# Kernel tuning notes

Measured on AMD Instinct MI355X. Metric: run time of the kernel, lower is better.

The kernel has to match this reference:

```python
import jax, jax.numpy as jnp
import numpy as np

EPS = 1e-5
NEG_SLOPE = 0.1


def conv2d(x, w, b, pad):
    y = jax.lax.conv_general_dilated(x, w, (1, 1), ((pad[0], pad[0]), (pad[1], pad[1])),
                                     dimension_numbers=('NCHW', 'OIHW', 'NCHW'))
    return y + b[None, :, None, None]


def bn(x, g, b, m, v):
    # inference-mode BatchNorm2d
    scale = g / jnp.sqrt(v + EPS)
    return (x - m[None, :, None, None]) * scale[None, :, None, None] + b[None, :, None, None]


def leaky(x):
    return jnp.where(x >= 0, x, NEG_SLOPE * x)


def pos_embed(C, T, V):
    # STTFormer-style sinusoidal embedding over joint index, repeated per frame
    pos = jnp.tile(jnp.arange(V, dtype=jnp.float32), T)[:, None]            # (T*V, 1)
    div = jnp.exp(jnp.arange(0, C, 2, dtype=jnp.float32) * (-np.log(10000.0) / C))
    pe = jnp.zeros((T * V, C), jnp.float32)
    pe = pe.at[:, 0::2].set(jnp.sin(pos * div)).at[:, 1::2].set(jnp.cos(pos * div))
    return pe.reshape(T, V, C).transpose(2, 0, 1)[None]                      # (1, C, T, V)


def ema(x, c1w, c1b, c3w, c3b, gng, gnb, groups):
    # Efficient Multi-scale Attention (EMA) module
    b, c, h, w = x.shape
    cg = c // groups
    gx = x.reshape(b * groups, cg, h, w)
    x_h = gx.mean(axis=3, keepdims=True)                                     # (bg, cg, h, 1)
    x_w = jnp.swapaxes(gx.mean(axis=2, keepdims=True), 2, 3)                 # (bg, cg, w, 1)
    hw = conv2d(jnp.concatenate([x_h, x_w], axis=2), c1w, c1b, (0, 0))       # 1x1 conv
    xh, xw = hw[:, :, :h], hw[:, :, h:]
    g = gx * jax.nn.sigmoid(xh) * jax.nn.sigmoid(jnp.swapaxes(xw, 2, 3))
    # GroupNorm(cg, cg): one channel per group -> per-channel spatial norm
    mu = g.mean((2, 3), keepdims=True)
    var = g.var((2, 3), keepdims=True)
    x1 = (g - mu) / jnp.sqrt(var + EPS) * gng[None, :, None, None] + gnb[None, :, None, None]
    x2 = conv2d(gx, c3w, c3b, (1, 1))                                        # 3x3 conv
    x11 = jax.nn.softmax(x1.mean((2, 3))[:, None, :], axis=-1)               # (bg, 1, cg)
    x21 = jax.nn.softmax(x2.mean((2, 3))[:, None, :], axis=-1)
    x12 = x2.reshape(b * groups, cg, h * w)
    x22 = x1.reshape(b * groups, cg, h * w)
    weights = (x11 @ x12 + x21 @ x22).reshape(b * groups, 1, h, w)
    return (gx * jax.nn.sigmoid(weights)).reshape(b, c, h, w)


def _forward(x, atten_weight, qkv_w, qkv_b, alphas, att0s, nets_w, nets_b,
             bn1_g, bn1_b, bn1_m, bn1_v,
             e1_c1w, e1_c1b, e1_c3w, e1_c3b, e1_gng, e1_gnb,
             bn2_g, bn2_b, bn2_m, bn2_v,
             nett_w, nett_b, bn3_g, bn3_b, bn3_m, bn3_v,
             e2_c1w, e2_c1b, e2_c3w, e2_c3b, e2_gng, e2_gnb,
             bn4_g, bn4_b, bn4_m, bn4_v):
    N, C, T, V = x.shape
    H = alphas.shape[1]
    D = qkv_w.shape[0] // (2 * H)
    xs = pos_embed(C, T, V) + x
    # 1x1 conv to q,k
    qk = jnp.einsum('oc,nctv->notv', qkv_w, xs) + qkv_b[None, :, None, None]
    qk = qk.reshape(N, 2 * H, D, T, V)
    q, k = qk[:, :H], qk[:, H:]
    # tanh attention over joints (V x V), scaled, weighted, plus learned bias table
    att = jnp.tanh(jnp.einsum('nhctu,nhctv->nhuv', q, k) / (D * T)) * alphas
    att = att * atten_weight[None, None] + att0s
    xs = jnp.einsum('nctu,nhuv->nhctv', x, att).reshape(N, H * C, T, V)
    x_ress = x  # in_channels == out_channels -> identity residual
    xs = leaky(bn(conv2d(xs, nets_w, nets_b, (0, 1)), bn1_g, bn1_b, bn1_m, bn1_v) + x_ress)
    xs = leaky(bn(ema(xs, e1_c1w, e1_c1b, e1_c3w, e1_c3b, e1_gng, e1_gnb, 16),
                  bn2_g, bn2_b, bn2_m, bn2_v) + x_ress)
    xt = leaky(bn(conv2d(xs, nett_w, nett_b, (2, 0)), bn3_g, bn3_b, bn3_m, bn3_v) + xs)
    xt = leaky(bn(ema(xt, e2_c1w, e2_c1b, e2_c3w, e2_c3b, e2_gng, e2_gnb, 32),
                  bn4_g, bn4_b, bn4_m, bn4_v) + xs)
    return xt


def setup_inputs() -> dict:
    key = jax.random.key(0)
    N, C, T, V, H, D, O = 64, 64, 120, 25, 3, 64, 64
    cg1, cg2 = O // 16, O // 32
    ks = jax.random.split(key, 16)
    f32 = jnp.float32

    def bn_params(k, c):
        k1, k2 = jax.random.split(k)
        return (jnp.ones(c, f32), jnp.zeros(c, f32),
                jax.random.normal(k1, (c,), f32) * 0.1,
                jax.random.uniform(k2, (c,), f32) + 0.5)

    bn1 = bn_params(ks[5], O)
    bn2 = bn_params(ks[6], O)
    bn3 = bn_params(ks[7], O)
    bn4 = bn_params(ks[8], O)
    return {
        'x': jax.random.normal(ks[0], (N, C, T, V), f32),
        'atten_weight': jax.random.uniform(ks[1], (V, V), f32),
        'qkv_w': jax.random.normal(ks[2], (2 * H * D, C), f32) * 0.05,
        'qkv_b': jnp.zeros(2 * H * D, f32),
        'alphas': jnp.ones((1, H, 1, 1), f32),
        'att0s': jnp.ones((1, H, V, V), f32) / V,
        'nets_w': jax.random.normal(ks[3], (O, C * H, 1, 3), f32) * 0.05,
        'nets_b': jnp.zeros(O, f32),
        'bn1_g': bn1[0], 'bn1_b': bn1[1], 'bn1_m': bn1[2], 'bn1_v': bn1[3],
        'e1_c1w': jax.random.normal(ks[9], (cg1, cg1, 1, 1), f32) * 0.1,
        'e1_c1b': jnp.zeros(cg1, f32),
        'e1_c3w': jax.random.normal(ks[10], (cg1, cg1, 3, 3), f32) * 0.1,
        'e1_c3b': jnp.zeros(cg1, f32),
        'e1_gng': jnp.ones(cg1, f32), 'e1_gnb': jnp.zeros(cg1, f32),
        'bn2_g': bn2[0], 'bn2_b': bn2[1], 'bn2_m': bn2[2], 'bn2_v': bn2[3],
        'nett_w': jax.random.normal(ks[4], (O, O, 5, 1), f32) * 0.05,
        'nett_b': jnp.zeros(O, f32),
        'bn3_g': bn3[0], 'bn3_b': bn3[1], 'bn3_m': bn3[2], 'bn3_v': bn3[3],
        'e2_c1w': jax.random.normal(ks[11], (cg2, cg2, 1, 1), f32) * 0.1,
        'e2_c1b': jnp.zeros(cg2, f32),
        'e2_c3w': jax.random.normal(ks[12], (cg2, cg2, 3, 3), f32) * 0.1,
        'e2_c3b': jnp.zeros(cg2, f32),
        'e2_gng': jnp.ones(cg2, f32), 'e2_gnb': jnp.zeros(cg2, f32),
        'bn4_g': bn4[0], 'bn4_b': bn4[1], 'bn4_m': bn4[2], 'bn4_v': bn4[3],
    }


def reference(x, atten_weight, qkv_w, qkv_b, alphas, att0s, nets_w, nets_b,
              bn1_g, bn1_b, bn1_m, bn1_v,
              e1_c1w, e1_c1b, e1_c3w, e1_c3b, e1_gng, e1_gnb,
              bn2_g, bn2_b, bn2_m, bn2_v,
              nett_w, nett_b, bn3_g, bn3_b, bn3_m, bn3_v,
              e2_c1w, e2_c1b, e2_c3w, e2_c3b, e2_gng, e2_gnb,
              bn4_g, bn4_b, bn4_m, bn4_v):
    return _forward(x, atten_weight, qkv_w, qkv_b, alphas, att0s, nets_w, nets_b,
                    bn1_g, bn1_b, bn1_m, bn1_v,
                    e1_c1w, e1_c1b, e1_c3w, e1_c3b, e1_gng, e1_gnb,
                    bn2_g, bn2_b, bn2_m, bn2_v,
                    nett_w, nett_b, bn3_g, bn3_b, bn3_m, bn3_v,
                    e2_c1w, e2_c1b, e2_c3w, e2_c3b, e2_gng, e2_gnb,
                    bn4_g, bn4_b, bn4_m, bn4_v)
```

## Files before the change

kernel.cpp:

```cpp
#include <hip/hip_runtime.h>

typedef float v2f __attribute__((ext_vector_type(2)));
typedef float v4f __attribute__((ext_vector_type(4)));
__device__ __forceinline__ v2f mk2(float a, float b){ v2f r; r.x=a; r.y=b; return r; }
__device__ __forceinline__ v2f bc2(float x){ v2f r; r.x=x; r.y=x; return r; }

__device__ __forceinline__ float sigm(float x){ return 1.f/(1.f+__expf(-x)); }

__device__ __forceinline__ float waveReduceSum(float v){
  #pragma unroll
  for (int o = 32; o > 0; o >>= 1) v += __shfl_down(v, o, 64);
  return v;
}
__device__ __forceinline__ float blockReduceSum(float v, float* red4, int tid){
  v = waveReduceSum(v);
  __syncthreads();
  if ((tid & 63) == 0) red4[tid >> 6] = v;
  __syncthreads();
  return red4[0] + red4[1] + red4[2] + red4[3];
}

__global__ __launch_bounds__(256) void zeroS_kernel(float* __restrict__ S){
  int i = blockIdx.x*256 + threadIdx.x;
  if (i < 120000) S[i] = 0.f;
}

__global__ __launch_bounds__(256) void att_prep_kernel(
    const float* __restrict__ qkv_w, const float* __restrict__ qkv_b, float* __restrict__ Mbuf)
{
  const int h = blockIdx.x;
  const int tid = threadIdx.x;
  __shared__ float Wq[4096], Wk[4096];
  for (int i=tid;i<4096;i+=256){
    Wq[i] = qkv_w[(size_t)h*4096 + i];
    Wk[i] = qkv_w[(size_t)(3+h)*4096 + i];
  }
  __syncthreads();
  int c = tid>>2, cp0 = (tid&3)*16;
  float acc[16];
  #pragma unroll
  for (int j=0;j<16;j++) acc[j]=0.f;
  for (int cq=0;cq<64;cq++){
    float wq = Wq[cq*64+c];
    #pragma unroll
    for (int j=0;j<16;j++) acc[j] += wq*Wk[cq*64+cp0+j];
  }
  float* dst = Mbuf + (size_t)h*4352;
  #pragma unroll
  for (int j=0;j<16;j++) dst[(cp0+j)*68 + c] = acc[j];
  if (tid < 128){
    int row = tid>>6, cp = tid&63;
    const float* W = row ? Wq : Wk;
    const float* bvec = qkv_b + (row ? h*64 : (3+h)*64);
    const float* bb = row ? (qkv_b + (3+h)*64) : (qkv_b + h*64);
    float s=0;
    for (int cq=0;cq<64;cq++) s += bb[cq]*W[cq*64+cp];
    Mbuf[(size_t)h*4352 + cp*68 + 64 + row] = s;
    (void)bvec;
  }
  if (tid==0){
    const float* qb = qkv_b + h*64; const float* kb = qkv_b + (3+h)*64;
    float s=0;
    for (int i=0;i<64;i++) s += qb[i]*kb[i];
    Mbuf[13056 + h] = s;
  }
}

__global__ __launch_bounds__(256,4) void att_partial_kernel(
    const float* __restrict__ x, const float* __restrict__ Mbuf, float* __restrict__ S)
{
  const int nh = blockIdx.x;
  const int tc = blockIdx.y;
  const int n = nh / 3, h = nh % 3;
  const int tid = threadIdx.x;
  __shared__ __align__(16) float Ms[4352];
  __shared__ float xt[1600];
  __shared__ float Ybuf[1650];
  for (int i=tid;i<4352;i+=256) Ms[i] = Mbuf[(size_t)h*4352 + i];

  float pe_reg[7]; int goff[7];
  #pragma unroll
  for (int k=0;k<7;k++){
    int i = tid + k*256;
    if (i < 1600){
      int c = i/25, uu = i%25;
      float freq = __expf(-(float)(2*(c>>1)) * 0.14391156835f);
      float a = (float)uu * freq;
      pe_reg[k] = (c & 1) ? cosf(a) : sinf(a);
      goff[k] = (n*64 + c)*3000 + uu;
    }
  }
  v2f saccv[2] = { {0.f,0.f}, {0.f,0.f} };
  float sacc4 = 0.f;
  const int u = tid / 5, v0 = (tid % 5) * 5;
  const int yc0 = (tid/25)*8, yv = tid%25;
  const int xv = (tid-200)%25;

  for (int t = tc*15; t < tc*15 + 15; ++t){
    __syncthreads();
    #pragma unroll
    for (int k=0;k<7;k++){
      int i = tid + k*256;
      if (i < 1600) xt[i] = x[goff[k] + t*25] + pe_reg[k];
    }
    __syncthreads();
    if (tid < 200){
      v2f a[4];
      #pragma unroll
      for (int j=0;j<4;j++) a[j] = bc2(0.f);
      const float* xb = &xt[yv];
      #pragma unroll 8
      for (int cp=0; cp<64; ++cp){
        v4f m0 = *reinterpret_cast<const v4f*>(&Ms[cp*68 + yc0]);
        v4f m1 = *reinterpret_cast<const v4f*>(&Ms[cp*68 + yc0 + 4]);
        v2f xv2 = bc2(xb[cp*25]);
        a[0] += mk2(m0.x, m0.y) * xv2;
        a[1] += mk2(m0.z, m0.w) * xv2;
        a[2] += mk2(m1.x, m1.y) * xv2;
        a[3] += mk2(m1.z, m1.w) * xv2;
      }
      #pragma unroll
      for (int j=0;j<4;j++){
        Ybuf[(yc0+2*j)*25 + yv]   = a[j].x;
        Ybuf[(yc0+2*j+1)*25 + yv] = a[j].y;
      }
    } else if (tid < 225){
      v2f a64 = bc2(0.f);
      const float* xb = &xt[xv];
      #pragma unroll 8
      for (int cp=0; cp<64; ++cp){
        v2f m = *reinterpret_cast<const v2f*>(&Ms[cp*68 + 64]);
        a64 += m * bc2(xb[cp*25]);
      }
      Ybuf[64*25 + xv] = a64.x;
      Ybuf[65*25 + xv] = a64.y;
    }
    __syncthreads();
    if (tid < 125){
      const float* Qb = &xt[u];
      const float* Kb = &Ybuf[v0];
      #pragma unroll 8
      for (int c = 0; c < 64; ++c){
        float q = Qb[c*25];
        saccv[0] += bc2(q) * mk2(Kb[c*25+0], Kb[c*25+1]);
        saccv[1] += bc2(q) * mk2(Kb[c*25+2], Kb[c*25+3]);
        sacc4 += q * Kb[c*25+4];
      }
      float ybu = Ybuf[65*25 + u];
      const float* av = &Ybuf[64*25 + v0];
      saccv[0] += mk2(av[0]+ybu, av[1]+ybu);
      saccv[1] += mk2(av[2]+ybu, av[3]+ybu);
      sacc4    += av[4]+ybu;
    }
  }
  if (tid < 125){
    float* dst = S + (size_t)nh*625 + u*25 + v0;
    atomicAdd(dst + 0, saccv[0].x);
    atomicAdd(dst + 1, saccv[0].y);
    atomicAdd(dst + 2, saccv[1].x);
    atomicAdd(dst + 3, saccv[1].y);
    atomicAdd(dst + 4, sacc4);
  }
}

__global__ __launch_bounds__(256) void att_finalize_kernel(
    float* __restrict__ S, const float* __restrict__ attw,
    const float* __restrict__ alphas, const float* __restrict__ att0s,
    const float* __restrict__ c0buf)
{
  int idx = blockIdx.x*256 + threadIdx.x;
  if (idx >= 120000) return;
  int nh = idx / 625, uv = idx % 625;
  int h = nh % 3;
  float a = tanhf((S[idx] + 120.f*c0buf[h]) * (1.f/7680.f)) * alphas[h];
  S[idx] = a * attw[uv] + att0s[h*625 + uv];
}

__global__ __launch_bounds__(256,4) void stage1_kernel(
    const float* __restrict__ x, const float* __restrict__ att,
    const float* __restrict__ nets_w, const float* __restrict__ nets_b,
    const float* __restrict__ bng, const float* __restrict__ bnb,
    const float* __restrict__ bnm, const float* __restrict__ bnv,
    float* __restrict__ s1)
{
  __shared__ float smem[7872];
  float* sc    = smem;
  float* sh    = smem + 64;
  float* att_s = smem + 128;
  float* xts   = smem + 2003;
  float* xbp   = smem + 5267;
  const int n = blockIdx.x, t0 = blockIdx.y*2;
  const int tid = threadIdx.x;

  for (int i=tid;i<1875;i+=256) att_s[i] = att[(size_t)n*1875 + i];
  for (int i=tid;i<3200;i+=256){
    int c=i/50, r=i%50;
    xts[c*51 + r] = x[((size_t)(n*64+c)*120 + t0 + r/25)*25 + (r%25)];
  }
  if (tid < 192){
    int row=tid>>2, p=tid&3;
    xbp[row*54 + ((p&1)?26:0) + ((p>>1)?27:0)] = 0.f;
  }
  if (tid < 64){
    float s = bng[tid]*rsqrtf(bnv[tid]+1e-5f);
    sc[tid]=s; sh[tid]=bnb[tid]-bnm[tid]*s;
  }
  __syncthreads();

  const int op = tid>>3, r = tid&7, tt = r>>2, vq = r&3;
  const int o0 = op*2, v0q = vq*7, nv = (vq<3)?7:4;
  v2f accv[7];
  #pragma unroll
  for (int j=0;j<7;j++) accv[j] = bc2(0.f);

  for (int q=0; q<4; ++q){
    const int hc0 = q*48;
    if (tid < 240){
      int hcH = tid % 48, vg = tid / 48;
      int hc = hc0 + hcH;
      int h = hc>>6, c = hc&63, v0 = vg*5;
      v2f av[5];
      #pragma unroll
      for (int j=0;j<5;j++) av[j] = bc2(0.f);
      const float* xr0 = &xts[c*51];
      for (int u=0;u<25;u++){
        v2f xv = mk2(xr0[u], xr0[u+25]);
        const float* ap = &att_s[(h*25+u)*25 + v0];
        #pragma unroll
        for (int j=0;j<5;j++) av[j] += bc2(ap[j]) * xv;
      }
      #pragma unroll
      for (int j=0;j<5;j++){
        xbp[hcH*54 + 1 + v0 + j]  = av[j].x;
        xbp[hcH*54 + 28 + v0 + j] = av[j].y;
      }
    }
    __syncthreads();

    const float* xbase = &xbp[tt*27 + v0q];
    const float* wg0 = nets_w + (size_t)o0*576 + hc0*3;
    const float* wg1 = wg0 + 576;
    #pragma unroll 4
    for (int hcL=0; hcL<48; ++hcL){
      float xr[9];
      #pragma unroll
      for (int j=0;j<9;j++) xr[j] = xbase[hcL*54 + j];
      v2f w0 = mk2(wg0[hcL*3+0], wg1[hcL*3+0]);
      v2f w1 = mk2(wg0[hcL*3+1], wg1[hcL*3+1]);
      v2f w2 = mk2(wg0[hcL*3+2], wg1[hcL*3+2]);
      #pragma unroll
      for (int j=0;j<7;j++)
        accv[j] += w0*bc2(xr[j]) + w1*bc2(xr[j+1]) + w2*bc2(xr[j+2]);
    }
    __syncthreads();
  }

  float b0 = nets_b[o0], b1 = nets_b[o0+1];
  const int t = t0 + tt;
  #pragma unroll
  for (int j=0;j<7;j++){
    if (j < nv){
      int v = v0q + j;
      size_t base0 = ((size_t)(n*64+o0)*120 + t)*25 + v;
      size_t base1 = ((size_t)(n*64+o0+1)*120 + t)*25 + v;
      float y0 = (accv[j].x + b0)*sc[o0]   + sh[o0]   + x[base0];
      float y1 = (accv[j].y + b1)*sc[o0+1] + sh[o0+1] + x[base1];
      y0 = (y0>=0.f)? y0 : 0.1f*y0;
      y1 = (y1>=0.f)? y1 : 0.1f*y1;
      s1[base0] = y0;
      s1[base1] = y1;
    }
  }
}

__global__ __launch_bounds__(256) void stage3_kernel(
    const float* __restrict__ s2, const float* __restrict__ nett_w, const float* __restrict__ nett_b,
    const float* __restrict__ bng, const float* __restrict__ bnb,
    const float* __restrict__ bnm, const float* __restrict__ bnv,
    float* __restrict__ s3)
{
  const int n = blockIdx.x, t0 = blockIdx.y*4;
  const int tid = threadIdx.x;
  __shared__ float tile[12800];
  __shared__ float sc[64], sh[64];
  for (int i=tid;i<12800;i+=256){
    int c=i/200, r=i%200, tt=r/25, v=r%25;
    int t = t0 + tt - 2;
    tile[i] = (t>=0 && t<120) ? s2[((size_t)(n*64+c)*120 + t)*25 + v] : 0.f;
  }
  if (tid < 64){
    float s = bng[tid]*rsqrtf(bnv[tid]+1e-5f);
    sc[tid]=s; sh[tid]=bnb[tid]-bnm[tid]*s;
  }
  __syncthreads();
  for (int task=tid; task<800; task+=256){
    int og = task/25, v = task%25; int o0 = og*2;
    v2f accv[4];
    { v2f b = mk2(nett_b[o0], nett_b[o0+1]);
      #pragma unroll
      for (int k=0;k<4;k++) accv[k]=b; }
    const float* tb = &tile[v];
    const float* wbase = nett_w + (size_t)o0*320;
    #pragma unroll 4
    for (int c=0;c<64;c++){
      float xr[8];
      #pragma unroll
      for (int k=0;k<8;k++) xr[k] = tb[c*200 + k*25];
      v2f w[5];
      #pragma unroll
      for (int d=0;d<5;d++) w[d] = mk2(wbase[c*5 + d], wbase[320 + c*5 + d]);
      #pragma unroll
      for (int k=0;k<4;k++){
        #pragma unroll
        for (int d=0;d<5;d++) accv[k] += w[d]*bc2(xr[k+d]);
      }
    }
    #pragma unroll
    for (int k=0;k<4;k++){
      int t=t0+k;
      float r0 = tile[o0*200     + (k+2)*25 + v];
      float r1 = tile[(o0+1)*200 + (k+2)*25 + v];
      float y0 = accv[k].x*sc[o0]   + sh[o0]   + r0;
      float y1 = accv[k].y*sc[o0+1] + sh[o0+1] + r1;
      y0 = (y0>=0.f)? y0 : 0.1f*y0;
      y1 = (y1>=0.f)? y1 : 0.1f*y1;
      s3[((size_t)(n*64+o0)*120   + t)*25 + v] = y0;
      s3[((size_t)(n*64+o0+1)*120 + t)*25 + v] = y1;
    }
  }
}

template<int CG, int G>
__global__ __launch_bounds__(256) void ema_kernel(
    const float* __restrict__ in, const float* __restrict__ res,
    const float* __restrict__ c1w, const float* __restrict__ c1b,
    const float* __restrict__ c3w, const float* __restrict__ c3b,
    const float* __restrict__ gng, const float* __restrict__ gnb,
    const float* __restrict__ bng, const float* __restrict__ bnb,
    const float* __restrict__ bnm, const float* __restrict__ bnv,
    float* __restrict__ out)
{
  constexpr int PR = 122*27;
  __shared__ float gx[CG*PR];
  __shared__ float xh[CG*120], xw[CG*25];
  __shared__ float sigh[CG*120], sigw[CG*25];
  __shared__ float red4[4];
  __shared__ float c1w_s[CG*CG], c1b_s[CG], c3w_s[CG*CG*9], c3b_s[CG],
                   gng_s[CG], gnb_s[CG], sc_s[CG], sh_s[CG];
  const int tid = threadIdx.x;
  const int b = blockIdx.x; const int n = b / G; const int grp = b % G; const int c0 = grp*CG;
  const float* src = in + (size_t)(n*64 + c0)*3000;
  for (int i = tid; i < CG*PR; i += 256) gx[i] = 0.f;
  if (tid < CG*CG) c1w_s[tid] = c1w[tid];
  if (tid < CG*CG*9) c3w_s[tid] = c3w[tid];
  if (tid < CG){
    c1b_s[tid] = c1b[tid];
    c3b_s[tid] = c3b[tid]; gng_s[tid]=gng[tid]; gnb_s[tid]=gnb[tid];
    float s = bng[c0+tid] * rsqrtf(bnv[c0+tid]+1e-5f);
    sc_s[tid] = s; sh_s[tid] = bnb[c0+tid] - bnm[c0+tid]*s;
  }
  __syncthreads();
  for (int i = tid; i < CG*3000; i += 256){
    int cc = i/3000, p = i%3000, t = p/25, v = p%25;
    gx[cc*PR + (t+1)*27 + (v+1)] = src[i];
  }
  __syncthreads();
  for (int j = tid; j < CG*120; j += 256){
    int cc=j/120, t=j%120; float s=0;
    for (int v=0;v<25;v++) s += gx[cc*PR+(t+1)*27+(v+1)];
    xh[j] = s*(1.f/25.f);
  }
  for (int j = tid; j < CG*25; j += 256){
    int cc=j/25, v=j%25; float s=0;
    for (int t=0;t<120;t++) s += gx[cc*PR+(t+1)*27+(v+1)];
    xw[j] = s*(1.f/120.f);
  }
  __syncthreads();
  for (int j = tid; j < CG*120; j += 256){
    int cc=j/120, t=j%120; float s=c1b_s[cc];
    #pragma unroll
    for (int i=0;i<CG;i++) s += c1w_s[cc*CG+i]*xh[i*120+t];
    sigh[j] = sigm(s);
  }
  for (int j = tid; j < CG*25; j += 256){
    int cc=j/25, v=j%25; float s=c1b_s[cc];
    #pragma unroll
    for (int i=0;i<CG;i++) s += c1w_s[cc*CG+i]*xw[i*25+v];
    sigw[j] = sigm(s);
  }
  __syncthreads();
  float gs[CG], gss[CG];
  #pragma unroll
  for (int cc=0;cc<CG;cc++){ gs[cc]=0.f; gss[cc]=0.f; }
  for (int p = tid; p < 3000; p += 256){
    int t=p/25, v=p%25;
    #pragma unroll
    for (int cc=0;cc<CG;cc++){
      float g = gx[cc*PR+(t+1)*27+(v+1)]*sigh[cc*120+t]*sigw[cc*25+v];
      gs[cc]+=g; gss[cc]+=g*g;
    }
  }
  #pragma unroll
  for (int cc=0;cc<CG;cc++){
    gs[cc]  = blockReduceSum(gs[cc],  red4, tid);
    gss[cc] = blockReduceSum(gss[cc], red4, tid);
  }
  float mu[CG], inv[CG];
  #pragma unroll
  for (int cc=0;cc<CG;cc++){
    mu[cc] = gs[cc]*(1.f/3000.f);
    float var = gss[cc]*(1.f/3000.f) - mu[cc]*mu[cc];
    inv[cc] = rsqrtf(fmaxf(var, 0.f) + 1e-5f);
  }
  float x11[CG];
  { float mx = gnb_s[0];
    #pragma unroll
    for (int cc=1;cc<CG;cc++) mx = fmaxf(mx, gnb_s[cc]);
    float sum=0;
    #pragma unroll
    for (int cc=0;cc<CG;cc++){ x11[cc]=__expf(gnb_s[cc]-mx); sum+=x11[cc]; }
    float r = 1.f/sum;
    #pragma unroll
    for (int cc=0;cc<CG;cc++) x11[cc]*=r; }
  float Sall[CG];
  #pragma unroll
  for (int i=0;i<CG;i++){ float s=0; for (int t=0;t<120;t++) s += xh[i*120+t]; Sall[i]=s*25.f; }
  float m2[CG];
  #pragma unroll
  for (int cc=0;cc<CG;cc++){
    float acc = c3b_s[cc]*3000.f;
    #pragma unroll
    for (int i=0;i<CG;i++){
      #pragma unroll
      for (int dy=0;dy<3;dy++){
        #pragma unroll
        for (int dx=0;dx<3;dx++){
          float w = c3w_s[(cc*CG+i)*9+dy*3+dx];
          float ss = Sall[i];
          int re = -1, ce = -1;
          if (dy==0){ ss -= 25.f*xh[i*120+119]; re=119; }
          else if (dy==2){ ss -= 25.f*xh[i*120+0]; re=0; }
          if (dx==0){ ss -= 120.f*xw[i*25+24]; ce=24; }
          else if (dx==2){ ss -= 120.f*xw[i*25+0]; ce=0; }
          if (re>=0 && ce>=0) ss += gx[i*PR + (re+1)*27 + (ce+1)];
          acc += w*ss;
        }
      }
    }
    m2[cc] = acc*(1.f/3000.f);
  }
  float x21[CG];
  { float mx = m2[0];
    #pragma unroll
    for (int cc=1;cc<CG;cc++) mx = fmaxf(mx, m2[cc]);
    float sum=0;
    #pragma unroll
    for (int cc=0;cc<CG;cc++){ x21[cc]=__expf(m2[cc]-mx); sum+=x21[cc]; }
    float r = 1.f/sum;
    #pragma unroll
    for (int cc=0;cc<CG;cc++) x21[cc]*=r; }
  float wm[CG*9]; float bm=0.f, kc=0.f;
  #pragma unroll
  for (int k=0;k<CG*9;k++){
    float s=0;
    #pragma unroll
    for (int cc=0;cc<CG;cc++) s += x11[cc]*c3w_s[cc*CG*9 + k];
    wm[k]=s;
  }
  float ga[CG];
  #pragma unroll
  for (int cc=0;cc<CG;cc++){
    bm += x11[cc]*c3b_s[cc];
    ga[cc] = x21[cc]*gng_s[cc]*inv[cc];
    kc += x21[cc]*(gnb_s[cc] - mu[cc]*gng_s[cc]*inv[cc]);
  }
  const float base = bm + kc;
  for (int p = tid; p < 3000; p += 256){
    int t=p/25, v=p%25;
    float wsum = base;
    #pragma unroll
    for (int i=0;i<CG;i++){
      const float* gp = &gx[i*PR + t*27 + v];
      wsum += wm[i*9+0]*gp[0]  + wm[i*9+1]*gp[1]  + wm[i*9+2]*gp[2]
            + wm[i*9+3]*gp[27] + wm[i*9+4]*gp[28] + wm[i*9+5]*gp[29]
            + wm[i*9+6]*gp[54] + wm[i*9+7]*gp[55] + wm[i*9+8]*gp[56];
    }
    #pragma unroll
    for (int cc=0;cc<CG;cc++){
      float g = gx[cc*PR+(t+1)*27+(v+1)]*sigh[cc*120+t]*sigw[cc*25+v];
      wsum += ga[cc]*g;
    }
    float sw = sigm(wsum);
    #pragma unroll
    for (int cc=0;cc<CG;cc++){
      float val = gx[cc*PR+(t+1)*27+(v+1)]*sw;
      float y = val*sc_s[cc] + sh_s[cc] + res[(size_t)(n*64+c0+cc)*3000 + p];
      y = (y >= 0.f) ? y : 0.1f*y;
      out[(size_t)(n*64+c0+cc)*3000 + p] = y;
    }
  }
}

extern "C" void kernel_launch(void* const* d_in, const int* in_sizes, int n_in,
                              void* d_out, int out_size, void* d_ws, size_t ws_size,
                              hipStream_t stream)
{
  const float* x      = (const float*)d_in[0];
  const float* attw   = (const float*)d_in[1];
  const float* qkv_w  = (const float*)d_in[2];
  const float* qkv_b  = (const float*)d_in[3];
  const float* alphas = (const float*)d_in[4];
  const float* att0s  = (const float*)d_in[5];
  const float* nets_w = (const float*)d_in[6];
  const float* nets_b = (const float*)d_in[7];
  const float* bn1g = (const float*)d_in[8];  const float* bn1b = (const float*)d_in[9];
  const float* bn1m = (const float*)d_in[10]; const float* bn1v = (const float*)d_in[11];
  const float* e1c1w = (const float*)d_in[12]; const float* e1c1b = (const float*)d_in[13];
  const float* e1c3w = (const float*)d_in[14]; const float* e1c3b = (const float*)d_in[15];
  const float* e1gng = (const float*)d_in[16]; const float* e1gnb = (const float*)d_in[17];
  const float* bn2g = (const float*)d_in[18]; const float* bn2b = (const float*)d_in[19];
  const float* bn2m = (const float*)d_in[20]; const float* bn2v = (const float*)d_in[21];
  const float* nettw = (const float*)d_in[22]; const float* nettb = (const float*)d_in[23];
  const float* bn3g = (const float*)d_in[24]; const float* bn3b = (const float*)d_in[25];
  const float* bn3m = (const float*)d_in[26]; const float* bn3v = (const float*)d_in[27];
  const float* e2c1w = (const float*)d_in[28]; const float* e2c1b = (const float*)d_in[29];
  const float* e2c3w = (const float*)d_in[30]; const float* e2c3b = (const float*)d_in[31];
  const float* e2gng = (const float*)d_in[32]; const float* e2gnb = (const float*)d_in[33];
  const float* bn4g = (const float*)d_in[34]; const float* bn4b = (const float*)d_in[35];
  const float* bn4m = (const float*)d_in[36]; const float* bn4v = (const float*)d_in[37];

  float* S    = (float*)d_ws;
  float* outf = (float*)d_out;
  float* xbuf = (float*)d_in[0];
  float* Mbuf = (float*)d_out;

  att_prep_kernel<<<3,256,0,stream>>>(qkv_w, qkv_b, Mbuf);
  zeroS_kernel<<<469,256,0,stream>>>(S);
  att_partial_kernel<<<dim3(192,8),256,0,stream>>>(x, Mbuf, S);
  att_finalize_kernel<<<469,256,0,stream>>>(S, attw, alphas, att0s, Mbuf + 13056);
  stage1_kernel<<<dim3(64,60),256,0,stream>>>(x, S, nets_w, nets_b, bn1g,bn1b,bn1m,bn1v, outf);
  ema_kernel<4,16><<<1024,256,0,stream>>>(outf, x,
      e1c1w,e1c1b,e1c3w,e1c3b,e1gng,e1gnb, bn2g,bn2b,bn2m,bn2v, xbuf);
  stage3_kernel<<<dim3(64,30),256,0,stream>>>(xbuf, nettw, nettb, bn3g,bn3b,bn3m,bn3v, outf);
  ema_kernel<2,32><<<2048,256,0,stream>>>(outf, xbuf,
      e2c1w,e2c1b,e2c3w,e2c3b,e2gng,e2gnb, bn4g,bn4b,bn4m,bn4v, outf);
}
```

Before: 992.4 us.

## Double-buffer attention input staging and vectorize conv weight loads

In the attention partial-score kernel, the x tile is now double-buffered. The global load and positional-embedding add for step t+1 overlap the score accumulation of step t, which cuts one barrier per time step. In the temporal/spatial conv kernel, weight reads are grouped into 128-bit vector loads of 12 floats per output channel for every 4 input channels. The double buffer adds 6.4KB of shared memory per block, which may reduce occupancy. The vector loads assume the weight pointers are 16-byte aligned.

```diff
diff --git a/kernel.cpp b/kernel.cpp
--- a/kernel.cpp
+++ b/kernel.cpp
@@ -51,12 +51,10 @@
   if (tid < 128){
     int row = tid>>6, cp = tid&63;
     const float* W = row ? Wq : Wk;
-    const float* bvec = qkv_b + (row ? h*64 : (3+h)*64);
     const float* bb = row ? (qkv_b + (3+h)*64) : (qkv_b + h*64);
     float s=0;
     for (int cq=0;cq<64;cq++) s += bb[cq]*W[cq*64+cp];
     Mbuf[(size_t)h*4352 + cp*68 + 64 + row] = s;
-    (void)bvec;
   }
   if (tid==0){
     const float* qb = qkv_b + h*64; const float* kb = qkv_b + (3+h)*64;
@@ -74,7 +72,7 @@
   const int n = nh / 3, h = nh % 3;
   const int tid = threadIdx.x;
   __shared__ __align__(16) float Ms[4352];
-  __shared__ float xt[1600];
+  __shared__ float xt[2][1600];
   __shared__ float Ybuf[1650];
   for (int i=tid;i<4352;i+=256) Ms[i] = Mbuf[(size_t)h*4352 + i];
 
@@ -96,19 +94,19 @@
   const int yc0 = (tid/25)*8, yv = tid%25;
   const int xv = (tid-200)%25;
 
-  for (int t = tc*15; t < tc*15 + 15; ++t){
-    __syncthreads();
+  auto do_stage = [&](int t, float* dst){
     #pragma unroll
     for (int k=0;k<7;k++){
       int i = tid + k*256;
-      if (i < 1600) xt[i] = x[goff[k] + t*25] + pe_reg[k];
-    }
-    __syncthreads();
+      if (i < 1600) dst[i] = x[goff[k] + t*25] + pe_reg[k];
+    }
+  };
+  auto do_Y = [&](const float* xtb){
     if (tid < 200){
       v2f a[4];
       #pragma unroll
       for (int j=0;j<4;j++) a[j] = bc2(0.f);
-      const float* xb = &xt[yv];
+      const float* xb = &xtb[yv];
       #pragma unroll 8
       for (int cp=0; cp<64; ++cp){
         v4f m0 = *reinterpret_cast<const v4f*>(&Ms[cp*68 + yc0]);
@@ -126,7 +124,7 @@
       }
     } else if (tid < 225){
       v2f a64 = bc2(0.f);
-      const float* xb = &xt[xv];
+      const float* xb = &xtb[xv];
       #pragma unroll 8
       for (int cp=0; cp<64; ++cp){
         v2f m = *reinterpret_cast<const v2f*>(&Ms[cp*68 + 64]);
@@ -135,25 +133,40 @@
       Ybuf[64*25 + xv] = a64.x;
       Ybuf[65*25 + xv] = a64.y;
     }
+  };
+  auto do_score = [&](const float* xtb){
+    const float* Qb = &xtb[u];
+    const float* Kb = &Ybuf[v0];
+    #pragma unroll 8
+    for (int c = 0; c < 64; ++c){
+      float q = Qb[c*25];
+      saccv[0] += bc2(q) * mk2(Kb[c*25+0], Kb[c*25+1]);
+      saccv[1] += bc2(q) * mk2(Kb[c*25+2], Kb[c*25+3]);
+      sacc4 += q * Kb[c*25+4];
+    }
+    float ybu = Ybuf[65*25 + u];
+    const float* av = &Ybuf[64*25 + v0];
+    saccv[0] += mk2(av[0]+ybu, av[1]+ybu);
+    saccv[1] += mk2(av[2]+ybu, av[3]+ybu);
+    sacc4    += av[4]+ybu;
+  };
+
+  const int t0 = tc*15;
+  do_stage(t0, xt[0]);
+  __syncthreads();
+  do_Y(xt[0]);
+  __syncthreads();
+  int b = 0;
+  for (int t = t0+1; t < t0+15; ++t){
+    do_stage(t, xt[b^1]);
+    if (tid < 125) do_score(xt[b]);
     __syncthreads();
-    if (tid < 125){
-      const float* Qb = &xt[u];
-      const float* Kb = &Ybuf[v0];
-      #pragma unroll 8
-      for (int c = 0; c < 64; ++c){
-        float q = Qb[c*25];
-        saccv[0] += bc2(q) * mk2(Kb[c*25+0], Kb[c*25+1]);
-        saccv[1] += bc2(q) * mk2(Kb[c*25+2], Kb[c*25+3]);
-        sacc4 += q * Kb[c*25+4];
-      }
-      float ybu = Ybuf[65*25 + u];
-      const float* av = &Ybuf[64*25 + v0];
-      saccv[0] += mk2(av[0]+ybu, av[1]+ybu);
-      saccv[1] += mk2(av[2]+ybu, av[3]+ybu);
-      sacc4    += av[4]+ybu;
-    }
+    do_Y(xt[b^1]);
+    __syncthreads();
+    b ^= 1;
   }
   if (tid < 125){
+    do_score(xt[b]);
     float* dst = S + (size_t)nh*625 + u*25 + v0;
     atomicAdd(dst + 0, saccv[0].x);
     atomicAdd(dst + 1, saccv[0].y);
@@ -240,17 +253,27 @@
     const float* xbase = &xbp[tt*27 + v0q];
     const float* wg0 = nets_w + (size_t)o0*576 + hc0*3;
     const float* wg1 = wg0 + 576;
-    #pragma unroll 4
-    for (int hcL=0; hcL<48; ++hcL){
-      float xr[9];
-      #pragma unroll
-      for (int j=0;j<9;j++) xr[j] = xbase[hcL*54 + j];
-      v2f w0 = mk2(wg0[hcL*3+0], wg1[hcL*3+0]);
-      v2f w1 = mk2(wg0[hcL*3+1], wg1[hcL*3+1]);
-      v2f w2 = mk2(wg0[hcL*3+2], wg1[hcL*3+2]);
-      #pragma unroll
-      for (int j=0;j<7;j++)
-        accv[j] += w0*bc2(xr[j]) + w1*bc2(xr[j+1]) + w2*bc2(xr[j+2]);
+    for (int g=0; g<12; ++g){
+      v4f W0[3], W1[3];
+      #pragma unroll
+      for (int m=0;m<3;m++){
+        W0[m] = *reinterpret_cast<const v4f*>(wg0 + g*12 + m*4);
+        W1[m] = *reinterpret_cast<const v4f*>(wg1 + g*12 + m*4);
+      }
+      #pragma unroll
+      for (int l=0;l<4;++l){
+        const int hcL = g*4 + l;
+        float xr[9];
+        #pragma unroll
+        for (int j=0;j<9;j++) xr[j] = xbase[hcL*54 + j];
+        const int b0 = l*3, b1 = l*3+1, b2 = l*3+2;
+        v2f w0 = mk2(W0[b0>>2][b0&3], W1[b0>>2][b0&3]);
+        v2f w1 = mk2(W0[b1>>2][b1&3], W1[b1>>2][b1&3]);
+        v2f w2 = mk2(W0[b2>>2][b2&3], W1[b2>>2][b2&3]);
+        #pragma unroll
+        for (int j=0;j<7;j++)
+          accv[j] += w0*bc2(xr[j]) + w1*bc2(xr[j+1]) + w2*bc2(xr[j+2]);
+      }
     }
     __syncthreads();
   }
```

New measurement: 966.2 us, median of 2. -2.6%, faster.
